# Kernel tuning notes

Hardware: AMD Instinct MI355X
Metric: run time of the kernel (lower is better)

Reference implementation:

```python
import jax, jax.numpy as jnp
import numpy as np

K = 5  # kernel_size per dim, dim=2 -> 25 kernel weights, degree-1 open B-splines


def _spline_basis(pseudo):
    """Degree-1 open B-spline basis for dim=2, kernel_size=5.
    pseudo: [E,2] in [0,1]. Returns basis [E,4], kernel index wi [E,4]."""
    v = pseudo * (K - 1)                      # [E,2]
    lo = jnp.floor(v)
    frac = v - lo                             # [E,2]
    lo = lo.astype(jnp.int32)
    b = jnp.stack([1.0 - frac, frac], axis=-1)            # [E,2,2] (edge, dim, offset)
    idx = jnp.clip(lo[..., None] + jnp.arange(2, dtype=jnp.int32), 0, K - 1)  # [E,2,2]
    basis = b[:, 0, :, None] * b[:, 1, None, :]           # [E,2,2]
    wi = idx[:, 0, :, None] + K * idx[:, 1, None, :]      # [E,2,2] (dim0 stride 1, dim1 stride K)
    E = pseudo.shape[0]
    return basis.reshape(E, 4), wi.reshape(E, 4)


def _spline_conv(x, src, dst, pseudo, W, root, bias, num_nodes):
    basis, wi = _spline_basis(pseudo)          # [E,4], [E,4]
    xW = jnp.einsum('ni,kio->nko', x, W)       # [N,25,out]
    gathered = xW[src[:, None], wi]            # [E,4,out]
    msg = jnp.einsum('es,eso->eo', basis, gathered)  # [E,out]
    agg = jax.ops.segment_max(msg, dst, num_segments=num_nodes)
    agg = jnp.where(jnp.isneginf(agg), 0.0, agg)  # empty segments -> 0 (PyG fill)
    return agg + x @ root + bias


def setup_inputs() -> dict:
    key = jax.random.key(0)
    ks = jax.random.split(key, 12)
    N, E, C = 50000, 800000, 64
    s = 1.0 / np.sqrt(C)
    return {
        'x': jax.random.normal(ks[0], (N, C), jnp.float32),
        'edge_index': jax.random.randint(ks[1], (2, E), 0, N, jnp.int32),
        'edge_attr': jax.random.uniform(ks[2], (E, 2), jnp.float32),
        'W1': jax.random.normal(ks[3], (25, C, C), jnp.float32) * s,
        'root1': jax.random.normal(ks[4], (C, C), jnp.float32) * s,
        'b1': jnp.zeros((C,), jnp.float32),
        'W2': jax.random.normal(ks[5], (25, C, C), jnp.float32) * s,
        'root2': jax.random.normal(ks[6], (C, C), jnp.float32) * s,
        'b2': jnp.zeros((C,), jnp.float32),
        'final_w': jax.random.normal(ks[7], (3 * C, C), jnp.float32) / np.sqrt(3 * C),
        'final_b': jnp.zeros((C,), jnp.float32),
    }


def reference(x, edge_index, edge_attr, W1, root1, b1, W2, root2, b2, final_w, final_b):
    N = x.shape[0]
    src, dst = edge_index[0], edge_index[1]
    x1 = jax.nn.relu(_spline_conv(x, src, dst, edge_attr, W1, root1, b1, N))
    x2 = jax.nn.relu(_spline_conv(x1, src, dst, edge_attr, W2, root2, b2, N))
    h = jnp.concatenate([x, x1, x2], axis=-1)   # cat=True; dropout p=0 (eval)
    return h @ final_w + final_b
```

## Files before the change

kernel.cpp:

```cpp
#include <hip/hip_runtime.h>
#include <hip/hip_bf16.h>


typedef short  bf16x8 __attribute__((ext_vector_type(8)));
typedef float  f32x4  __attribute__((ext_vector_type(4)));
typedef int    i32x4  __attribute__((ext_vector_type(4)));
typedef ushort u16x8  __attribute__((ext_vector_type(8)));

__device__ __forceinline__ float bf2f(ushort u) {
    return __uint_as_float((uint)u << 16);
}
__device__ __forceinline__ ushort f2bf(float f) {
    uint u = __float_as_uint(f);
    return (ushort)((u + 0x7FFF + ((u >> 16) & 1)) >> 16);
}

__global__ __launch_bounds__(256) void prep(
    const float* __restrict__ x, ushort* __restrict__ xb, int nx8,
    const float* __restrict__ W1, const float* __restrict__ r1, ushort* __restrict__ WtA,
    const float* __restrict__ W2, const float* __restrict__ r2, ushort* __restrict__ WtB,
    const float* __restrict__ fw, ushort* __restrict__ fwT,
    int* __restrict__ deg, int N)
{
    const int nw = 26 * 4096, nfw = 3 * 4096;
    int idx = blockIdx.x * 256 + threadIdx.x;
    if (idx < nx8) {
        float4 v0 = *(const float4*)(x + (size_t)idx * 8);
        float4 v1 = *(const float4*)(x + (size_t)idx * 8 + 4);
        u16x8 o;
        o[0] = f2bf(v0.x); o[1] = f2bf(v0.y); o[2] = f2bf(v0.z); o[3] = f2bf(v0.w);
        o[4] = f2bf(v1.x); o[5] = f2bf(v1.y); o[6] = f2bf(v1.z); o[7] = f2bf(v1.w);
        *(u16x8*)(xb + (size_t)idx * 8) = o;
        return;
    }
    idx -= nx8;
    if (idx < nw) {
        int tile = idx >> 12, rem = idx & 4095, o = rem >> 6, i = rem & 63;
        WtA[idx] = f2bf(tile < 25 ? W1[tile * 4096 + i * 64 + o] : r1[i * 64 + o]);
        return;
    }
    idx -= nw;
    if (idx < nw) {
        int tile = idx >> 12, rem = idx & 4095, o = rem >> 6, i = rem & 63;
        WtB[idx] = f2bf(tile < 25 ? W2[tile * 4096 + i * 64 + o] : r2[i * 64 + o]);
        return;
    }
    idx -= nw;
    if (idx < nfw) {
        int t = idx >> 12, rem = idx & 4095, o = rem >> 6, k = rem & 63;
        fwT[idx] = f2bf(fw[(t * 64 + k) * 64 + o]);
        return;
    }
    idx -= nfw;
    if (idx < N) deg[idx] = 0;
}

__global__ __launch_bounds__(256) void hist_deg(
    const int* __restrict__ ei, int* __restrict__ deg, int E)
{
    int e = blockIdx.x * 256 + threadIdx.x;
    if (e < E) atomicAdd(&deg[ei[E + e]], 1);
}

__global__ __launch_bounds__(1024) void scan_block(
    const int* __restrict__ deg, int* __restrict__ inc,
    int* __restrict__ partial, int N)
{
    __shared__ int s[1024];
    int i = blockIdx.x * 1024 + threadIdx.x;
    int v = (i < N) ? deg[i] : 0;
    s[threadIdx.x] = v;
    __syncthreads();
    for (int off = 1; off < 1024; off <<= 1) {
        int t = (threadIdx.x >= off) ? s[threadIdx.x - off] : 0;
        __syncthreads();
        s[threadIdx.x] += t;
        __syncthreads();
    }
    if (i < N) inc[i] = s[threadIdx.x];
    if (threadIdx.x == 1023) partial[blockIdx.x] = s[1023];
}

__global__ void scan_partial(int* __restrict__ partial, int nb)
{
    __shared__ int s[64];
    int t = threadIdx.x;
    int v = (t < nb) ? partial[t] : 0;
    s[t] = v;
    __syncthreads();
    for (int off = 1; off < 64; off <<= 1) {
        int x = (t >= off) ? s[t - off] : 0;
        __syncthreads();
        s[t] += x;
        __syncthreads();
    }
    if (t < nb) partial[t] = s[t] - v;
}

__global__ __launch_bounds__(1024) void scan_finalize(
    const int* __restrict__ deg, const int* __restrict__ inc,
    const int* __restrict__ partial, int* __restrict__ row_ptr,
    int* __restrict__ cursor, int N)
{
    int i = blockIdx.x * 1024 + threadIdx.x;
    if (i >= N) return;
    int v = inc[i] + partial[blockIdx.x];
    row_ptr[i + 1] = v;
    cursor[i] = v - deg[i];
    if (i == 0) row_ptr[0] = 0;
}

__global__ __launch_bounds__(256) void gemm_scatter(
    const ushort* __restrict__ A, const ushort* __restrict__ Wt,
    ushort* __restrict__ xWb, ushort* __restrict__ xRoot, int mtiles,
    const int* __restrict__ ei, const float* __restrict__ attr,
    int* __restrict__ cursor, int4* __restrict__ epack, int E)
{
    __shared__ ushort Cs[4][16][72];
    const int bx = blockIdx.x;

    if (bx >= 26) {
        if (!ei) return;
        int e = ((bx - 26) * gridDim.y + blockIdx.y) * 256 + threadIdx.x;
        if (e >= E) return;
        int src = ei[e], dst = ei[E + e];
        float u = attr[2 * e] * 4.f;
        float v = attr[2 * e + 1] * 4.f;
        float lu = floorf(u), lv = floorf(v);
        float fu = u - lu, fv = v - lv;
        int iu = (int)lu;  iu = iu < 0 ? 0 : (iu > 4 ? 4 : iu);
        int iv = (int)lv;  iv = iv < 0 ? 0 : (iv > 4 ? 4 : iv);
        int iu1 = iu + 1 > 4 ? 4 : iu + 1;
        int iv1 = iv + 1 > 4 ? 4 : iv + 1;
        uint slots = (uint)(iu + 5 * iv) | ((uint)(iu + 5 * iv1) << 8) |
                     ((uint)(iu1 + 5 * iv) << 16) | ((uint)(iu1 + 5 * iv1) << 24);
        uint wlo = (uint)f2bf((1.f - fu) * (1.f - fv)) | ((uint)f2bf((1.f - fu) * fv) << 16);
        uint whi = (uint)f2bf(fu * (1.f - fv)) | ((uint)f2bf(fu * fv) << 16);
        int pos = atomicAdd(&cursor[dst], 1);
        i32x4 pk = {src * 3200, (int)slots, (int)wlo, (int)whi};
        __builtin_nontemporal_store(pk, (i32x4*)(epack + pos));
        return;
    }

    const int wave = threadIdx.x >> 6;
    const int lane = threadIdx.x & 63;
    const int l16 = lane & 15;
    const int half = lane >> 4;
    ushort (*cw)[72] = Cs[wave];

    const ushort* btile = Wt + (size_t)bx * 4096;
    bf16x8 b0[4], b1[4];
    #pragma unroll
    for (int s = 0; s < 4; ++s) {
        const ushort* brow = btile + (size_t)(s * 16 + l16) * 64;
        b0[s] = *(const bf16x8*)(brow + half * 8);
        b1[s] = *(const bf16x8*)(brow + 32 + half * 8);
    }

    const int mt_base = blockIdx.y * 8;
    const int nit = (mtiles - mt_base) < 8 ? (mtiles - mt_base) : 8;

    const ushort* arow0 = A + (size_t)(mt_base * 64 + wave * 16 + l16) * 64;
    bf16x8 a0 = *(const bf16x8*)(arow0 + half * 8);
    bf16x8 a1 = *(const bf16x8*)(arow0 + 32 + half * 8);

    for (int it = 0; it < nit; ++it) {
        const int m0 = (mt_base + it) * 64;
        const int m_base = m0 + wave * 16;

        bf16x8 na0, na1;
        if (it + 1 < nit) {
            const ushort* arow = A + (size_t)(m_base + 64 + l16) * 64;
            na0 = *(const bf16x8*)(arow + half * 8);
            na1 = *(const bf16x8*)(arow + 32 + half * 8);
        }

        f32x4 acc[4];
        #pragma unroll
        for (int s = 0; s < 4; ++s) {
            acc[s] = (f32x4){0.f, 0.f, 0.f, 0.f};
            acc[s] = __builtin_amdgcn_mfma_f32_16x16x32_bf16(a0, b0[s], acc[s], 0, 0, 0);
            acc[s] = __builtin_amdgcn_mfma_f32_16x16x32_bf16(a1, b1[s], acc[s], 0, 0, 0);
        }

        if (bx == 25) {
            #pragma unroll
            for (int s = 0; s < 4; ++s)
                #pragma unroll
                for (int r = 0; r < 4; ++r)
                    xRoot[(size_t)(m_base + half * 4 + r) * 64 + s * 16 + l16] = f2bf(acc[s][r]);
        } else {
            #pragma unroll
            for (int s = 0; s < 4; ++s)
                #pragma unroll
                for (int r = 0; r < 4; ++r)
                    cw[half * 4 + r][s * 16 + l16] = f2bf(acc[s][r]);
            #pragma unroll
            for (int i2 = 0; i2 < 2; ++i2) {
                int idx = i2 * 64 + lane;
                int row = idx >> 3, seg = idx & 7;
                uint4 v = *(const uint4*)&cw[row][seg * 8];
                *(uint4*)(xWb + (size_t)(m_base + row) * 1600 + bx * 64 + seg * 8) = v;
            }
        }
        a0 = na0; a1 = na1;
    }
}

__device__ __forceinline__ void gather4(
    const char* __restrict__ xwb, int lane, int rb, uint slots, ushort g[4])
{
    g[0] = *((const ushort*)(xwb + rb + ((slots & 255u) << 7)) + lane);
    g[1] = *((const ushort*)(xwb + rb + (((slots >> 8) & 255u) << 7)) + lane);
    g[2] = *((const ushort*)(xwb + rb + (((slots >> 16) & 255u) << 7)) + lane);
    g[3] = *((const ushort*)(xwb + rb + ((slots >> 24) << 7)) + lane);
}

__device__ __forceinline__ float consume4(const int4 d, const ushort g[4])
{
    float m = __uint_as_float((uint)d.z << 16) * bf2f(g[0]);
    m = fmaf(__uint_as_float((uint)d.z & 0xffff0000u), bf2f(g[1]), m);
    m = fmaf(__uint_as_float((uint)d.w << 16), bf2f(g[2]), m);
    m = fmaf(__uint_as_float((uint)d.w & 0xffff0000u), bf2f(g[3]), m);
    return m;
}

__global__ __launch_bounds__(256) void edge_csr(
    const ushort* __restrict__ xWb, const int* __restrict__ row_ptr,
    const int4* __restrict__ epack, const ushort* __restrict__ xRoot,
    const float* __restrict__ bias, float* __restrict__ outf,
    ushort* __restrict__ outb, int N)
{
    const int wv = __builtin_amdgcn_readfirstlane(threadIdx.x >> 6);
    const int d = blockIdx.x * 4 + wv;
    const int lane = threadIdx.x & 63;
    if (d >= N) return;
    const int e0 = __builtin_amdgcn_readfirstlane(row_ptr[d]);
    const int e1 = __builtin_amdgcn_readfirstlane(row_ptr[d + 1]);
    const char* xwb = (const char*)xWb;
    const int cnt = e1 - e0;

    float vmax = -__builtin_inff();
    int e = e0;
    const int quads = cnt >> 2;
    if (quads > 0) {
        int4 dq[4]; ushort gq[4][4];
        #pragma unroll
        for (int j = 0; j < 4; ++j) {
            dq[j] = epack[e + j];
            gather4(xwb, lane, dq[j].x, (uint)dq[j].y, gq[j]);
        }
        for (int q = 1; q < quads; ++q) {
            int4 nd[4]; ushort ng[4][4];
            #pragma unroll
            for (int j = 0; j < 4; ++j) {
                nd[j] = epack[e + 4 * q + j];
                gather4(xwb, lane, nd[j].x, (uint)nd[j].y, ng[j]);
            }
            #pragma unroll
            for (int j = 0; j < 4; ++j)
                vmax = fmaxf(vmax, consume4(dq[j], gq[j]));
            #pragma unroll
            for (int j = 0; j < 4; ++j) {
                dq[j] = nd[j];
                #pragma unroll
                for (int i = 0; i < 4; ++i) gq[j][i] = ng[j][i];
            }
        }
        #pragma unroll
        for (int j = 0; j < 4; ++j)
            vmax = fmaxf(vmax, consume4(dq[j], gq[j]));
        e += quads * 4;
    }
    for (; e < e1; ++e) {
        int4 dA = epack[e];
        ushort gA[4];
        gather4(xwb, lane, dA.x, (uint)dA.y, gA);
        vmax = fmaxf(vmax, consume4(dA, gA));
    }
    if (cnt == 0) vmax = 0.f;
    float val = vmax + bf2f(xRoot[(size_t)d * 64 + lane]) + bias[lane];
    val = fmaxf(val, 0.f);
    if (outf) outf[(size_t)d * 64 + lane] = val;
    if (outb) outb[(size_t)d * 64 + lane] = f2bf(val);
}

__global__ __launch_bounds__(256) void final_mfma(
    const ushort* __restrict__ xb, const ushort* __restrict__ x1b,
    const ushort* __restrict__ x2b, const ushort* __restrict__ fwT,
    const float* __restrict__ fb, float* __restrict__ out, int M)
{
    const int wave = threadIdx.x >> 6;
    const int lane = threadIdx.x & 63;
    const int l16 = lane & 15;
    const int half = lane >> 4;
    const int m_base = blockIdx.x * 64 + wave * 16;
    const ushort* srcs[3] = {xb, x1b, x2b};

    f32x4 acc[4];
    #pragma unroll
    for (int s = 0; s < 4; ++s) acc[s] = (f32x4){0.f, 0.f, 0.f, 0.f};

    #pragma unroll
    for (int t = 0; t < 3; ++t) {
        const ushort* arow = srcs[t] + (size_t)(m_base + l16) * 64;
        bf16x8 a0 = *(const bf16x8*)(arow + half * 8);
        bf16x8 a1 = *(const bf16x8*)(arow + 32 + half * 8);
        const ushort* btile = fwT + (size_t)t * 4096;
        #pragma unroll
        for (int s = 0; s < 4; ++s) {
            const ushort* brow = btile + (size_t)(s * 16 + l16) * 64;
            bf16x8 b0 = *(const bf16x8*)(brow + half * 8);
            bf16x8 b1 = *(const bf16x8*)(brow + 32 + half * 8);
            acc[s] = __builtin_amdgcn_mfma_f32_16x16x32_bf16(a0, b0, acc[s], 0, 0, 0);
            acc[s] = __builtin_amdgcn_mfma_f32_16x16x32_bf16(a1, b1, acc[s], 0, 0, 0);
        }
    }

    #pragma unroll
    for (int s = 0; s < 4; ++s) {
        int o = s * 16 + l16;
        float b = fb[o];
        #pragma unroll
        for (int r = 0; r < 4; ++r) {
            int m = m_base + half * 4 + r;
            if (m < M) out[(size_t)m * 64 + o] = acc[s][r] + b;
        }
    }
}

extern "C" void kernel_launch(void* const* d_in, const int* in_sizes, int n_in,
                              void* d_out, int out_size, void* d_ws, size_t ws_size,
                              hipStream_t stream)
{
    const float* x    = (const float*)d_in[0];
    const int*   ei   = (const int*)d_in[1];
    const float* attr = (const float*)d_in[2];
    const float* W1   = (const float*)d_in[3];
    const float* r1   = (const float*)d_in[4];
    const float* b1   = (const float*)d_in[5];
    const float* W2   = (const float*)d_in[6];
    const float* r2   = (const float*)d_in[7];
    const float* b2   = (const float*)d_in[8];
    const float* fw   = (const float*)d_in[9];
    const float* fb   = (const float*)d_in[10];
    float* out = (float*)d_out;

    const int N = in_sizes[0] / 64;
    const int E = in_sizes[1] / 2;
    const int mtiles = (N + 63) / 64;
    const int Npad = mtiles * 64;

    char* p = (char*)d_ws;
    auto alloc = [&](size_t bytes) { void* q = p; p += (bytes + 255) & ~(size_t)255; return q; };
    int4*   epack  = (int4*)alloc((size_t)E * 16);
    ushort* xRoot  = (ushort*)alloc((size_t)Npad * 64 * 2);
    ushort* xWb    = (ushort*)alloc((size_t)Npad * 1600 * 2);
    ushort* xb     = (ushort*)alloc((size_t)Npad * 64 * 2);
    ushort* x1b    = (ushort*)alloc((size_t)Npad * 64 * 2);
    ushort* x2b    = (ushort*)alloc((size_t)Npad * 64 * 2);
    ushort* WtA    = (ushort*)alloc((size_t)26 * 4096 * 2);
    ushort* WtB    = (ushort*)alloc((size_t)26 * 4096 * 2);
    ushort* fwT    = (ushort*)alloc((size_t)3 * 4096 * 2);
    int*    deg    = (int*)alloc((size_t)N * 4);
    int*    cursor = (int*)alloc((size_t)N * 4);
    int*    rowp   = (int*)alloc((size_t)(N + 1) * 4);
    int*    tmpinc = (int*)alloc((size_t)N * 4);
    int*    part   = (int*)alloc(64 * 4);

    const int nb = (N + 1023) / 1024;

    const int nx8 = N * 8;
    const int nprep = nx8 + 2 * 26 * 4096 + 3 * 4096 + N;
    prep<<<(nprep + 255) / 256, 256, 0, stream>>>(
        x, xb, nx8, W1, r1, WtA, W2, r2, WtB, fw, fwT, deg, N);

    hist_deg<<<(E + 255) / 256, 256, 0, stream>>>(ei, deg, E);
    scan_block<<<nb, 1024, 0, stream>>>(deg, tmpinc, part, N);
    scan_partial<<<1, 64, 0, stream>>>(part, nb);
    scan_finalize<<<nb, 1024, 0, stream>>>(deg, tmpinc, part, rowp, cursor, N);

    const int gy = (mtiles + 7) / 8;
    const int sc_blocks = (E + 255) / 256;
    const int sc_cols = (sc_blocks + gy - 1) / gy;

    gemm_scatter<<<dim3(26 + sc_cols, gy), 256, 0, stream>>>(
        xb, WtA, xWb, xRoot, mtiles, ei, attr, cursor, epack, E);
    edge_csr<<<(N + 3) / 4, 256, 0, stream>>>(xWb, rowp, epack, xRoot, b1, nullptr, x1b, N);

    gemm_scatter<<<dim3(26, gy), 256, 0, stream>>>(
        x1b, WtB, xWb, xRoot, mtiles, nullptr, nullptr, nullptr, nullptr, E);
    edge_csr<<<(N + 3) / 4, 256, 0, stream>>>(xWb, rowp, epack, xRoot, b2, nullptr, x2b, N);

    final_mfma<<<mtiles, 256, 0, stream>>>(xb, x1b, x2b, fwT, fb, out, N);
}
```

Baseline: 380.1 us.

## Process two destination nodes per wave in edge gather and fold degree histogram into prep

```diff
diff --git a/kernel.cpp b/kernel.cpp
--- a/kernel.cpp
+++ b/kernel.cpp
@@ -20,7 +20,7 @@
     const float* __restrict__ W1, const float* __restrict__ r1, ushort* __restrict__ WtA,
     const float* __restrict__ W2, const float* __restrict__ r2, ushort* __restrict__ WtB,
     const float* __restrict__ fw, ushort* __restrict__ fwT,
-    int* __restrict__ deg, int N)
+    const int* __restrict__ ei, int* __restrict__ deg, int E)
 {
     const int nw = 26 * 4096, nfw = 3 * 4096;
     int idx = blockIdx.x * 256 + threadIdx.x;
@@ -52,14 +52,7 @@
         return;
     }
     idx -= nfw;
-    if (idx < N) deg[idx] = 0;
-}
-
-__global__ __launch_bounds__(256) void hist_deg(
-    const int* __restrict__ ei, int* __restrict__ deg, int E)
-{
-    int e = blockIdx.x * 256 + threadIdx.x;
-    if (e < E) atomicAdd(&deg[ei[E + e]], 1);
+    if (idx < E) atomicAdd(&deg[ei[E + idx]], 1);
 }
 
 __global__ __launch_bounds__(1024) void scan_block(
@@ -228,61 +221,108 @@
 __global__ __launch_bounds__(256) void edge_csr(
     const ushort* __restrict__ xWb, const int* __restrict__ row_ptr,
     const int4* __restrict__ epack, const ushort* __restrict__ xRoot,
-    const float* __restrict__ bias, float* __restrict__ outf,
-    ushort* __restrict__ outb, int N)
+    const float* __restrict__ bias, ushort* __restrict__ outb, int N)
 {
     const int wv = __builtin_amdgcn_readfirstlane(threadIdx.x >> 6);
-    const int d = blockIdx.x * 4 + wv;
     const int lane = threadIdx.x & 63;
-    if (d >= N) return;
-    const int e0 = __builtin_amdgcn_readfirstlane(row_ptr[d]);
-    const int e1 = __builtin_amdgcn_readfirstlane(row_ptr[d + 1]);
+    const int dA = blockIdx.x * 8 + wv * 2;
+    if (dA >= N) return;
+    const int dB = dA + 1;
+    const bool hasB = dB < N;
     const char* xwb = (const char*)xWb;
-    const int cnt = e1 - e0;
-
-    float vmax = -__builtin_inff();
-    int e = e0;
-    const int quads = cnt >> 2;
-    if (quads > 0) {
-        int4 dq[4]; ushort gq[4][4];
+
+    const int a0 = __builtin_amdgcn_readfirstlane(row_ptr[dA]);
+    const int a1 = __builtin_amdgcn_readfirstlane(row_ptr[dA + 1]);
+    const int b0 = hasB ? __builtin_amdgcn_readfirstlane(row_ptr[dB]) : 0;
+    const int b1 = hasB ? __builtin_amdgcn_readfirstlane(row_ptr[dB + 1]) : 0;
+    const int cntA = a1 - a0, cntB = b1 - b0;
+    const int qA = cntA >> 2, qB = cntB >> 2;
+    const int qmax = qA > qB ? qA : qB;
+
+    float vmA = -__builtin_inff(), vmB = -__builtin_inff();
+    int4 dqA[4], dqB[4];
+    ushort gqA[4][4], gqB[4][4];
+
+    if (qA > 0) {
         #pragma unroll
         for (int j = 0; j < 4; ++j) {
-            dq[j] = epack[e + j];
-            gather4(xwb, lane, dq[j].x, (uint)dq[j].y, gq[j]);
-        }
-        for (int q = 1; q < quads; ++q) {
-            int4 nd[4]; ushort ng[4][4];
+            dqA[j] = epack[a0 + j];
+            gather4(xwb, lane, dqA[j].x, (uint)dqA[j].y, gqA[j]);
+        }
+    }
+    if (qB > 0) {
+        #pragma unroll
+        for (int j = 0; j < 4; ++j) {
+            dqB[j] = epack[b0 + j];
+            gather4(xwb, lane, dqB[j].x, (uint)dqB[j].y, gqB[j]);
+        }
+    }
+
+    for (int q = 0; q < qmax; ++q) {
+        int4 ndA[4], ndB[4];
+        ushort ngA[4][4], ngB[4][4];
+        const bool pA = (q + 1 < qA), pB = (q + 1 < qB);
+        if (pA) {
             #pragma unroll
             for (int j = 0; j < 4; ++j) {
-                nd[j] = epack[e + 4 * q + j];
-                gather4(xwb, lane, nd[j].x, (uint)nd[j].y, ng[j]);
+                ndA[j] = epack[a0 + 4 * (q + 1) + j];
+                gather4(xwb, lane, ndA[j].x, (uint)ndA[j].y, ngA[j]);
             }
-            #pragma unroll
-            for (int j = 0; j < 4; ++j)
-                vmax = fmaxf(vmax, consume4(dq[j], gq[j]));
+        }
+        if (pB) {
             #pragma unroll
             for (int j = 0; j < 4; ++j) {
-                dq[j] = nd[j];
+                ndB[j] = epack[b0 + 4 * (q + 1) + j];
+                gather4(xwb, lane, ndB[j].x, (uint)ndB[j].y, ngB[j]);
+            }
+        }
+        if (q < qA) {
+            #pragma unroll
+            for (int j = 0; j < 4; ++j) vmA = fmaxf(vmA, consume4(dqA[j], gqA[j]));
+        }
+        if (q < qB) {
+            #pragma unroll
+            for (int j = 0; j < 4; ++j) vmB = fmaxf(vmB, consume4(dqB[j], gqB[j]));
+        }
+        if (pA) {
+            #pragma unroll
+            for (int j = 0; j < 4; ++j) {
+                dqA[j] = ndA[j];
                 #pragma unroll
-                for (int i = 0; i < 4; ++i) gq[j][i] = ng[j][i];
+                for (int i = 0; i < 4; ++i) gqA[j][i] = ngA[j][i];
             }
         }
-        #pragma unroll
-        for (int j = 0; j < 4; ++j)
-            vmax = fmaxf(vmax, consume4(dq[j], gq[j]));
-        e += quads * 4;
-    }
-    for (; e < e1; ++e) {
-        int4 dA = epack[e];
-        ushort gA[4];
-        gather4(xwb, lane, dA.x, (uint)dA.y, gA);
-        vmax = fmaxf(vmax, consume4(dA, gA));
-    }
-    if (cnt == 0) vmax = 0.f;
-    float val = vmax + bf2f(xRoot[(size_t)d * 64 + lane]) + bias[lane];
-    val = fmaxf(val, 0.f);
-    if (outf) outf[(size_t)d * 64 + lane] = val;
-    if (outb) outb[(size_t)d * 64 + lane] = f2bf(val);
+        if (pB) {
+            #pragma unroll
+            for (int j = 0; j < 4; ++j) {
+                dqB[j] = ndB[j];
+                #pragma unroll
+                for (int i = 0; i < 4; ++i) gqB[j][i] = ngB[j][i];
+            }
+        }
+    }
+
+    for (int e = a0 + qA * 4; e < a1; ++e) {
+        int4 d = epack[e];
+        ushort g[4];
+        gather4(xwb, lane, d.x, (uint)d.y, g);
+        vmA = fmaxf(vmA, consume4(d, g));
+    }
+    for (int e = b0 + qB * 4; e < b1; ++e) {
+        int4 d = epack[e];
+        ushort g[4];
+        gather4(xwb, lane, d.x, (uint)d.y, g);
+        vmB = fmaxf(vmB, consume4(d, g));
+    }
+
+    if (cntA == 0) vmA = 0.f;
+    float valA = vmA + bf2f(xRoot[(size_t)dA * 64 + lane]) + bias[lane];
+    outb[(size_t)dA * 64 + lane] = f2bf(fmaxf(valA, 0.f));
+    if (hasB) {
+        if (cntB == 0) vmB = 0.f;
+        float valB = vmB + bf2f(xRoot[(size_t)dB * 64 + lane]) + bias[lane];
+        outb[(size_t)dB * 64 + lane] = f2bf(fmaxf(valB, 0.f));
+    }
 }
 
 __global__ __launch_bounds__(256) void final_mfma(
@@ -370,12 +410,12 @@
 
     const int nb = (N + 1023) / 1024;
 
+    hipMemsetAsync(deg, 0, (size_t)N * 4, stream);
     const int nx8 = N * 8;
-    const int nprep = nx8 + 2 * 26 * 4096 + 3 * 4096 + N;
+    const int nprep = nx8 + 2 * 26 * 4096 + 3 * 4096 + E;
     prep<<<(nprep + 255) / 256, 256, 0, stream>>>(
-        x, xb, nx8, W1, r1, WtA, W2, r2, WtB, fw, fwT, deg, N);
-
-    hist_deg<<<(E + 255) / 256, 256, 0, stream>>>(ei, deg, E);
+        x, xb, nx8, W1, r1, WtA, W2, r2, WtB, fw, fwT, ei, deg, E);
+
     scan_block<<<nb, 1024, 0, stream>>>(deg, tmpinc, part, N);
     scan_partial<<<1, 64, 0, stream>>>(part, nb);
     scan_finalize<<<nb, 1024, 0, stream>>>(deg, tmpinc, part, rowp, cursor, N);
@@ -386,11 +426,11 @@
 
     gemm_scatter<<<dim3(26 + sc_cols, gy), 256, 0, stream>>>(
         xb, WtA, xWb, xRoot, mtiles, ei, attr, cursor, epack, E);
-    edge_csr<<<(N + 3) / 4, 256, 0, stream>>>(xWb, rowp, epack, xRoot, b1, nullptr, x1b, N);
+    edge_csr<<<(N + 7) / 8, 256, 0, stream>>>(xWb, rowp, epack, xRoot, b1, x1b, N);
 
     gemm_scatter<<<dim3(26, gy), 256, 0, stream>>>(
         x1b, WtB, xWb, xRoot, mtiles, nullptr, nullptr, nullptr, nullptr, E);
-    edge_csr<<<(N + 3) / 4, 256, 0, stream>>>(xWb, rowp, epack, xRoot, b2, nullptr, x2b, N);
+    edge_csr<<<(N + 7) / 8, 256, 0, stream>>>(xWb, rowp, epack, xRoot, b2, x2b, N);
 
     final_mfma<<<mtiles, 256, 0, stream>>>(xb, x1b, x2b, fwT, fb, out, N);
 }
```

After: 383.9 us. About the same (+1.0%).
